# Kernel tuning notes

Hardware: AMD Instinct MI355X
Metric: run time of the kernel (lower is better)

Reference implementation:

```python
import jax, jax.numpy as jnp
import numpy as np

THRESH = 0.6
PRIOR_ITER = 12800
PRIOR_RATE = 1.0
COORD_RATE = 1.0
NOOBJ_RATE = 1.0
OBJECT_RATE = 5.0
CLASS_RATE = 1.0
ANCHORS_NP = np.array([[1.3221/13, 1.73145/13], [3.19275/13, 4.00944/13],
                       [5.05587/13, 8.09892/13], [9.47112/13, 4.84053/13],
                       [11.2364/13, 10.0071/13]], dtype=np.float32)
B, H, W, A, C, T = 32, 38, 38, 5, 80, 60


def setup_inputs() -> dict:
    key = jax.random.key(0)
    k1, k2, k3, k4 = jax.random.split(key, 4)
    output = jax.random.normal(k1, (B, H, W, A * (5 + C)), dtype=jnp.float32)
    # well-formed ground-truth boxes: corners (x1,y1,x2,y2) in (0,1), x1<x2, y1<y2
    cxy = jax.random.uniform(k2, (B, T, 2), minval=0.05, maxval=0.95)
    wh = jax.random.uniform(k3, (B, T, 2), minval=0.02, maxval=0.4)
    x1y1 = jnp.clip(cxy - wh / 2, 0.001, 0.998)
    x2y2 = jnp.clip(cxy + wh / 2, 0.002, 0.999)
    cls = jax.random.randint(k4, (B, T, 1), 0, C).astype(jnp.float32)
    truths = jnp.concatenate([x1y1, x2y2, cls], axis=-1)
    return {"output": output, "truths": truths,
            "anchors": jnp.asarray(ANCHORS_NP), "iteration": 5000}


def _pair_iou(b1, b2):
    # b1: [B, N, 4], b2: [B, M, 4] corner boxes -> IOU [B, N, M]
    a1 = (b1[..., 2] - b1[..., 0]) * (b1[..., 3] - b1[..., 1])
    a2 = (b2[..., 2] - b2[..., 0]) * (b2[..., 3] - b2[..., 1])
    xmax = jnp.minimum(b1[..., 2][:, :, None], b2[..., 2][:, None, :])
    xmin = jnp.maximum(b1[..., 0][:, :, None], b2[..., 0][:, None, :])
    ymax = jnp.minimum(b1[..., 3][:, :, None], b2[..., 3][:, None, :])
    ymin = jnp.maximum(b1[..., 1][:, :, None], b2[..., 1][:, None, :])
    inter = jnp.clip(xmax - xmin, 0.0) * jnp.clip(ymax - ymin, 0.0)
    union = jnp.clip(a1[:, :, None] + a2[:, None, :] - inter, 1e-12)
    return inter / union


def yolo_loss(output, truths, anchors, iteration):
    Bs, Hs, Ws, TN = output.shape
    An = anchors.shape[0]
    Cn = TN // An - 5
    Tn = truths.shape[1]
    HW = Hs * Ws
    preds = output.reshape(Bs, HW, An, 5 + Cn)
    pred_t = preds[..., :5]           # raw tx,ty,tw,th,tconf
    pred_class = preds[..., 5:]
    gy, gx = jnp.meshgrid(jnp.arange(Hs), jnp.arange(Ws), indexing='ij')  # hw index = h*W + w
    gx = gx.reshape(-1).astype(output.dtype)
    gy = gy.reshape(-1).astype(output.dtype)
    cx = (jax.nn.sigmoid(pred_t[..., 0]) + gx[None, :, None]) / Ws
    cy = (jax.nn.sigmoid(pred_t[..., 1]) + gy[None, :, None]) / Hs
    pwh = jnp.exp(pred_t[..., 2:4]) * anchors[None, None]  # [B,HW,A,2]
    pred_boxes = jnp.stack([cx - pwh[..., 0] / 2, cy - pwh[..., 1] / 2,
                            cx + pwh[..., 0] / 2, cy + pwh[..., 1] / 2], axis=-1)
    # ---------- target assignment (torch.no_grad block) ----------
    tb = jax.lax.stop_gradient(truths)
    anc = jax.lax.stop_gradient(anchors)
    pb = jax.lax.stop_gradient(pred_boxes).reshape(Bs, HW * An, 4)
    t_c = (tb[..., 0:2] + tb[..., 2:4]) / 2.0
    t_wh = tb[..., 2:4] - tb[..., 0:2]
    tdx = t_c[..., 0] * Ws
    tdy = t_c[..., 1] * Hs
    gxt = jnp.ceil(tdx) - 1.0
    gyt = jnp.ceil(tdy) - 1.0
    ddx = -jnp.log(1.0 / (tdx - gxt) - 1.0)   # reverse sigmoid
    ddy = -jnp.log(1.0 / (tdy - gyt) - 1.0)
    # noobj: every predicted box whose best IOU vs any truth < thresh
    ious = _pair_iou(pb, tb[..., 0:4])        # [B, HW*A, T]
    noobj_cand = (ious.max(axis=2) < THRESH).reshape(Bs, HW, An)
    # anchor matching: IOU of origin-centered truth box vs origin-centered anchors
    iw = jnp.minimum(t_wh[..., 0:1], anc[None, None, :, 0])
    ih = jnp.minimum(t_wh[..., 1:2], anc[None, None, :, 1])
    inter = iw * ih
    union = jnp.clip(t_wh[..., 0:1] * t_wh[..., 1:2] +
                     (anc[:, 0] * anc[:, 1])[None, None] - inter, 1e-12)
    ta_iou = inter / union                    # [B, T, A]
    best_iou = ta_iou.max(axis=2)
    best_a = jnp.argmax(ta_iou, axis=2)       # first max index, matches torch
    pos = (gyt * Ws + gxt).astype(jnp.int32)  # [B, T]
    bidx = jnp.broadcast_to(jnp.arange(Bs, dtype=jnp.int32)[:, None], (Bs, Tn))
    # conflict resolution: sequential overwrite-if-strictly-better == per-cell
    # winner is max-IOU truth, earliest index on ties
    keys = (bidx * HW + pos) * An + best_a.astype(jnp.int32)
    kf = keys.reshape(-1)
    iouf = best_iou.reshape(-1)
    nseg = Bs * HW * An
    seg_best = jax.ops.segment_max(iouf, kf, num_segments=nseg)
    is_best = iouf == seg_best[kf]
    order = jnp.arange(Bs * Tn, dtype=jnp.int32)
    first = jax.ops.segment_min(jnp.where(is_best, order, Bs * Tn), kf, num_segments=nseg)
    win = is_best & (order == first[kf]) & (iouf > 0)
    af = best_a.reshape(-1)
    wh_t = jnp.log(t_wh.reshape(-1, 2)) / anc[af]   # faithful: log(wh)/anchor
    onehot = jax.nn.one_hot(tb[..., 4].reshape(-1).astype(jnp.int32), Cn, dtype=output.dtype)
    vals = jnp.concatenate([ddx.reshape(-1, 1), ddy.reshape(-1, 1), wh_t,
                            iouf[:, None], onehot], axis=1)  # [B*T, 5+C]
    vals = jnp.where(win[:, None], vals, 0.0)
    size_vals = jnp.where(win[:, None], t_wh.reshape(-1, 2), 0.0)
    bf = bidx.reshape(-1)
    pf = pos.reshape(-1)
    truth_resp = jnp.zeros((Bs, HW, An, 5 + Cn), output.dtype).at[bf, pf, af].add(vals)
    resp_cnt = jnp.zeros((Bs, HW, An), output.dtype).at[bf, pf, af].add(win.astype(output.dtype))
    truth_size = jnp.zeros((Bs, HW, An, 2), output.dtype).at[bf, pf, af].add(size_vals)
    mask_resp = resp_cnt > 0
    mask_noobj = (~mask_resp) & noobj_cand
    # ---------- losses (sum-reduced MSE over masked elements) ----------
    fix = jnp.sqrt(2.0 - truth_size[..., 0] * truth_size[..., 1])[..., None]
    loss_coord = COORD_RATE * jnp.sum(jnp.where(
        mask_resp[..., None], (fix * (pred_t[..., 0:4] - truth_resp[..., 0:4])) ** 2, 0.0))
    loss_object = OBJECT_RATE * jnp.sum(jnp.where(
        mask_resp, (pred_t[..., 4] - truth_resp[..., 4]) ** 2, 0.0))
    loss_class = CLASS_RATE * jnp.sum(jnp.where(
        mask_resp[..., None], (pred_class - truth_resp[..., 5:]) ** 2, 0.0))
    loss_noobj = NOOBJ_RATE * jnp.sum(jnp.where(mask_noobj, pred_t[..., 4] ** 2, 0.0))
    if iteration < PRIOR_ITER:
        loss_prior = PRIOR_RATE * jnp.sum((pwh - anchors[None, None]) ** 2)
    else:
        loss_prior = jnp.asarray(0.0, output.dtype)
    return (loss_noobj + loss_prior + loss_coord + loss_object + loss_class) / Bs


def reference(output, truths, anchors, iteration):
    return yolo_loss(output, truths, anchors, iteration)
```

## Files before the change

kernel.cpp:

```cpp
#include <hip/hip_runtime.h>
#include <math.h>

namespace {
constexpr int kB = 32;
constexpr int kH = 38;
constexpr int kW = 38;
constexpr int kA = 5;
constexpr int kC = 80;
constexpr int kT = 60;
constexpr int kHW = kH * kW;
constexpr int kCellsPerB = kHW * kA;
constexpr int kChan = 5 + kC;
constexpr int kMainBlocks = (kCellsPerB + 255) / 256;
constexpr int kTotalBlocks = kMainBlocks * kB;
constexpr int kPriorIter = 12800;
constexpr float kQ = 0.6f / 1.6f;
constexpr unsigned int kMagic = 0x9E3779B9u;
}

__global__ __launch_bounds__(256) void yolo_main_kernel(
    const float* __restrict__ output,
    const float* __restrict__ truths,
    const float* __restrict__ anchors,
    const int* __restrict__ iter_p,
    unsigned long long* __restrict__ words,
    float* __restrict__ out) {
  const int b = blockIdx.y;
  const int base = blockIdx.x * 256;
  const int idx = base + threadIdx.x;

  __shared__ float4 sbox[kT];
  __shared__ float4 stgt[kT];
  __shared__ float2 sfxc[kT];
  __shared__ unsigned long long swin[256];
  __shared__ float sanch[2 * kA];
  __shared__ float wsum[4];
  __shared__ float rs[256];

  swin[threadIdx.x] = 0ULL;
  if (threadIdx.x < 2 * kA) sanch[threadIdx.x] = anchors[threadIdx.x];
  __syncthreads();

  if (threadIdx.x < kT) {
    const int t = threadIdx.x;
    const float* tr = truths + (size_t)(b * kT + t) * 5;
    const float x1 = tr[0], y1 = tr[1], x2 = tr[2], y2 = tr[3], cls = tr[4];
    const float tw = x2 - x1, th = y2 - y1, tarea = tw * th;
    sbox[t] = make_float4(x1, y1, x2, y2);
    const float tdx = (x1 + x2) * 0.5f * (float)kW;
    const float tdy = (y1 + y2) * 0.5f * (float)kH;
    const float cxf = ceilf(tdx), cyf = ceilf(tdy);
    int gxi = (int)cxf - 1, gyi = (int)cyf - 1;
    gxi = min(max(gxi, 0), kW - 1);
    gyi = min(max(gyi, 0), kH - 1);
    float best = -1.0f;
    int ba = 0;
    for (int a2 = 0; a2 < kA; ++a2) {
      const float aw = anchors[2 * a2], ah = anchors[2 * a2 + 1];
      const float inter = fminf(tw, aw) * fminf(th, ah);
      const float uni = fmaxf(tarea + aw * ah - inter, 1e-12f);
      const float iou = inter / uni;
      if (iou > best) { best = iou; ba = a2; }
    }
    const int key = (gyi * kW + gxi) * kA + ba;
    const int local = key - base;
    if (local >= 0 && local < 256 && best > 0.0f) {
      const unsigned long long pk =
          ((unsigned long long)__float_as_uint(best) << 32) |
          (unsigned long long)(0xFFFFFFFFu - (unsigned int)t);
      atomicMax(&swin[local], pk);
    }
    const float fxr = tdx - (cxf - 1.0f);
    const float fyr = tdy - (cyf - 1.0f);
    stgt[t] = make_float4(-logf(1.0f / fxr - 1.0f),
                          -logf(1.0f / fyr - 1.0f),
                          logf(tw) / anchors[2 * ba],
                          logf(th) / anchors[2 * ba + 1]);
    sfxc[t] = make_float2(2.0f - tarea, __int_as_float((int)cls));
  }
  __syncthreads();

  const bool priorOn = (*iter_p < kPriorIter);
  float contrib = 0.0f;

  if (idx < kCellsPerB) {
    const int hw = idx / kA;
    const int a = idx - hw * kA;
    const int gx = hw % kW;
    const int gy = hw / kW;
    const float* p = output + (size_t)(b * kCellsPerB + idx) * kChan;
    const float4 tv = *(const float4*)p;
    const float t4 = p[4];
    const float t0 = tv.x, t1 = tv.y, t2 = tv.z, t3 = tv.w;
    const float aw = sanch[2 * a], ah = sanch[2 * a + 1];

    const float sx = __builtin_amdgcn_rcpf(1.0f + __expf(-t0));
    const float sy = __builtin_amdgcn_rcpf(1.0f + __expf(-t1));
    const float cx = (sx + (float)gx) * (1.0f / (float)kW);
    const float cy = (sy + (float)gy) * (1.0f / (float)kH);
    const float pw = __expf(t2) * aw;
    const float ph = __expf(t3) * ah;
    const float px1 = cx - pw * 0.5f, px2 = cx + pw * 0.5f;
    const float py1 = cy - ph * 0.5f, py2 = cy + ph * 0.5f;
    const float c0 = kQ * ((px2 - px1) * (py2 - py1));

    float mviol = -1.0f;
    for (int t = 0; t < kT; ++t) {
      const float4 bx = sbox[t];
      const float xm = fmaxf(px1, bx.x), xM = fminf(px2, bx.z);
      const float ym = fmaxf(py1, bx.y), yM = fminf(py2, bx.w);
      const float inter = fmaxf(xM - xm, 0.0f) * fmaxf(yM - ym, 0.0f);
      const float tarea = (bx.z - bx.x) * (bx.w - bx.y);
      mviol = fmaxf(mviol, inter - fmaf(kQ, tarea, c0));
    }

    if (priorOn) {
      const float dw = pw - aw, dh = ph - ah;
      contrib += dw * dw + dh * dh;
    }

    const unsigned long long pk = swin[threadIdx.x];
    if (pk != 0ULL) {
      const int t = (int)(0xFFFFFFFFu - (unsigned int)(pk & 0xFFFFFFFFULL));
      const float bi = __uint_as_float((unsigned int)(pk >> 32));
      const float4 tg = stgt[t];
      const float2 fc = sfxc[t];
      const float d0 = t0 - tg.x, d1 = t1 - tg.y;
      const float d2 = t2 - tg.z, d3 = t3 - tg.w;
      contrib += fc.x * (d0 * d0 + d1 * d1 + d2 * d2 + d3 * d3);
      const float dob = t4 - bi;
      contrib += 5.0f * dob * dob;
      const int cls = __float_as_int(fc.y);
      const float4* pc4 = (const float4*)(p + 5);
      float cs = 0.0f;
#pragma unroll
      for (int c = 0; c < kC / 4; ++c) {
        const float4 v = pc4[c];
        cs += v.x * v.x + v.y * v.y + v.z * v.z + v.w * v.w;
      }
      contrib += cs + 1.0f - 2.0f * p[5 + cls];
    } else if (mviol < 0.0f) {
      contrib += t4 * t4;
    }
  }

  for (int off = 32; off > 0; off >>= 1) contrib += __shfl_down(contrib, off);
  const int lane = threadIdx.x & 63;
  const int wid = threadIdx.x >> 6;
  if (lane == 0) wsum[wid] = contrib;
  __syncthreads();
  if (threadIdx.x == 0) {
    const float blockSum = wsum[0] + wsum[1] + wsum[2] + wsum[3];
    const unsigned long long word =
        ((unsigned long long)kMagic << 32) |
        (unsigned long long)__float_as_uint(blockSum);
    __hip_atomic_store(&words[b * kMainBlocks + blockIdx.x], word,
                       __ATOMIC_RELAXED, __HIP_MEMORY_SCOPE_AGENT);
  }

  if (blockIdx.x == 0 && blockIdx.y == 0) {
    float v = 0.0f;
    for (int j = threadIdx.x; j < kTotalBlocks; j += 256) {
      unsigned long long w;
      for (;;) {
        w = __hip_atomic_load(&words[j], __ATOMIC_RELAXED,
                              __HIP_MEMORY_SCOPE_AGENT);
        if ((unsigned int)(w >> 32) == kMagic) break;
        __builtin_amdgcn_s_sleep(1);
      }
      v += __uint_as_float((unsigned int)(w & 0xFFFFFFFFULL));
    }
    rs[threadIdx.x] = v;
    __syncthreads();
    for (int off = 128; off > 0; off >>= 1) {
      if (threadIdx.x < off) rs[threadIdx.x] += rs[threadIdx.x + off];
      __syncthreads();
    }
    if (threadIdx.x == 0) out[0] = rs[0] * (1.0f / (float)kB);
  }
}

extern "C" void kernel_launch(void* const* d_in, const int* in_sizes, int n_in,
                              void* d_out, int out_size, void* d_ws, size_t ws_size,
                              hipStream_t stream) {
  const float* output  = (const float*)d_in[0];
  const float* truths  = (const float*)d_in[1];
  const float* anchors = (const float*)d_in[2];
  const int*   iter_p  = (const int*)d_in[3];
  float* out = (float*)d_out;
  unsigned long long* words = (unsigned long long*)d_ws;

  hipLaunchKernelGGL(yolo_main_kernel, dim3(kMainBlocks, kB), dim3(256), 0,
                     stream, output, truths, anchors, iter_p, words, out);
}
```

Before: 20.22 us.

## Split IoU scan across two threads per cell and hoist prediction loads

Each cell is now handled by a pair of threads: each scans half of the 60 truth boxes and the two partial maxima are combined with a lane-xor shuffle. Blocks cover 128 cells instead of 256, which doubles the block count and the number of words the final reducer must poll. The raw prediction load is moved ahead of the shared-memory setup so its latency overlaps the truth preprocessing. The cost is duplicated sigmoid/exp work per pair, a larger final reduction, and idle odd lanes during the responsible-cell class loop.

```diff
diff --git a/kernel.cpp b/kernel.cpp
--- a/kernel.cpp
+++ b/kernel.cpp
@@ -11,7 +11,8 @@
 constexpr int kHW = kH * kW;
 constexpr int kCellsPerB = kHW * kA;
 constexpr int kChan = 5 + kC;
-constexpr int kMainBlocks = (kCellsPerB + 255) / 256;
+constexpr int kCellsPerBlk = 128;
+constexpr int kMainBlocks = (kCellsPerB + kCellsPerBlk - 1) / kCellsPerBlk;
 constexpr int kTotalBlocks = kMainBlocks * kB;
 constexpr int kPriorIter = 12800;
 constexpr float kQ = 0.6f / 1.6f;
@@ -26,18 +27,28 @@
     unsigned long long* __restrict__ words,
     float* __restrict__ out) {
   const int b = blockIdx.y;
-  const int base = blockIdx.x * 256;
-  const int idx = base + threadIdx.x;
+  const int base = blockIdx.x * kCellsPerBlk;
+  const int cell = base + (threadIdx.x >> 1);
+  const int half = threadIdx.x & 1;
+  const bool valid = cell < kCellsPerB;
 
   __shared__ float4 sbox[kT];
   __shared__ float4 stgt[kT];
   __shared__ float2 sfxc[kT];
-  __shared__ unsigned long long swin[256];
+  __shared__ unsigned long long swin[kCellsPerBlk];
   __shared__ float sanch[2 * kA];
   __shared__ float wsum[4];
   __shared__ float rs[256];
 
-  swin[threadIdx.x] = 0ULL;
+  float4 tv = make_float4(0.f, 0.f, 0.f, 0.f);
+  float t4 = 0.f;
+  const float* p = output + (size_t)(b * kCellsPerB + (valid ? cell : 0)) * kChan;
+  if (valid) {
+    tv = *(const float4*)p;
+    t4 = p[4];
+  }
+
+  if (threadIdx.x < kCellsPerBlk) swin[threadIdx.x] = 0ULL;
   if (threadIdx.x < 2 * kA) sanch[threadIdx.x] = anchors[threadIdx.x];
   __syncthreads();
 
@@ -64,7 +75,7 @@
     }
     const int key = (gyi * kW + gxi) * kA + ba;
     const int local = key - base;
-    if (local >= 0 && local < 256 && best > 0.0f) {
+    if (local >= 0 && local < kCellsPerBlk && best > 0.0f) {
       const unsigned long long pk =
           ((unsigned long long)__float_as_uint(best) << 32) |
           (unsigned long long)(0xFFFFFFFFu - (unsigned int)t);
@@ -83,14 +94,11 @@
   const bool priorOn = (*iter_p < kPriorIter);
   float contrib = 0.0f;
 
-  if (idx < kCellsPerB) {
-    const int hw = idx / kA;
-    const int a = idx - hw * kA;
+  if (valid) {
+    const int hw = cell / kA;
+    const int a = cell - hw * kA;
     const int gx = hw % kW;
     const int gy = hw / kW;
-    const float* p = output + (size_t)(b * kCellsPerB + idx) * kChan;
-    const float4 tv = *(const float4*)p;
-    const float t4 = p[4];
     const float t0 = tv.x, t1 = tv.y, t2 = tv.z, t3 = tv.w;
     const float aw = sanch[2 * a], ah = sanch[2 * a + 1];
 
@@ -105,42 +113,45 @@
     const float c0 = kQ * ((px2 - px1) * (py2 - py1));
 
     float mviol = -1.0f;
-    for (int t = 0; t < kT; ++t) {
-      const float4 bx = sbox[t];
+    const int ts = half * (kT / 2);
+    for (int k = 0; k < kT / 2; ++k) {
+      const float4 bx = sbox[ts + k];
       const float xm = fmaxf(px1, bx.x), xM = fminf(px2, bx.z);
       const float ym = fmaxf(py1, bx.y), yM = fminf(py2, bx.w);
       const float inter = fmaxf(xM - xm, 0.0f) * fmaxf(yM - ym, 0.0f);
       const float tarea = (bx.z - bx.x) * (bx.w - bx.y);
       mviol = fmaxf(mviol, inter - fmaf(kQ, tarea, c0));
     }
-
-    if (priorOn) {
-      const float dw = pw - aw, dh = ph - ah;
-      contrib += dw * dw + dh * dh;
-    }
-
-    const unsigned long long pk = swin[threadIdx.x];
-    if (pk != 0ULL) {
-      const int t = (int)(0xFFFFFFFFu - (unsigned int)(pk & 0xFFFFFFFFULL));
-      const float bi = __uint_as_float((unsigned int)(pk >> 32));
-      const float4 tg = stgt[t];
-      const float2 fc = sfxc[t];
-      const float d0 = t0 - tg.x, d1 = t1 - tg.y;
-      const float d2 = t2 - tg.z, d3 = t3 - tg.w;
-      contrib += fc.x * (d0 * d0 + d1 * d1 + d2 * d2 + d3 * d3);
-      const float dob = t4 - bi;
-      contrib += 5.0f * dob * dob;
-      const int cls = __float_as_int(fc.y);
-      const float4* pc4 = (const float4*)(p + 5);
-      float cs = 0.0f;
+    mviol = fmaxf(mviol, __shfl_xor(mviol, 1));
+
+    if (half == 0) {
+      if (priorOn) {
+        const float dw = pw - aw, dh = ph - ah;
+        contrib += dw * dw + dh * dh;
+      }
+      const unsigned long long pk = swin[threadIdx.x >> 1];
+      if (pk != 0ULL) {
+        const int t = (int)(0xFFFFFFFFu - (unsigned int)(pk & 0xFFFFFFFFULL));
+        const float bi = __uint_as_float((unsigned int)(pk >> 32));
+        const float4 tg = stgt[t];
+        const float2 fc = sfxc[t];
+        const float d0 = t0 - tg.x, d1 = t1 - tg.y;
+        const float d2 = t2 - tg.z, d3 = t3 - tg.w;
+        contrib += fc.x * (d0 * d0 + d1 * d1 + d2 * d2 + d3 * d3);
+        const float dob = t4 - bi;
+        contrib += 5.0f * dob * dob;
+        const int cls = __float_as_int(fc.y);
+        const float4* pc4 = (const float4*)(p + 5);
+        float cs = 0.0f;
 #pragma unroll
-      for (int c = 0; c < kC / 4; ++c) {
-        const float4 v = pc4[c];
-        cs += v.x * v.x + v.y * v.y + v.z * v.z + v.w * v.w;
+        for (int c = 0; c < kC / 4; ++c) {
+          const float4 v = pc4[c];
+          cs += v.x * v.x + v.y * v.y + v.z * v.z + v.w * v.w;
+        }
+        contrib += cs + 1.0f - 2.0f * p[5 + cls];
+      } else if (mviol < 0.0f) {
+        contrib += t4 * t4;
       }
-      contrib += cs + 1.0f - 2.0f * p[5 + cls];
-    } else if (mviol < 0.0f) {
-      contrib += t4 * t4;
     }
   }
 
```

Result: faster. 17.68 us (-12.6%).
